# Kernel tuning notes

Measured on AMD Instinct MI355X. Metric: run time of the kernel, lower is better.

## Reference

```python
import jax, jax.numpy as jnp
import numpy as np

N = 50000      # nodes
E = 800000     # edges (before self-loops)
F_IN = 128     # args.nsegment
H = 4          # args.nhead
C = 32         # args.dhidden
OUT = 64       # output_dim
G = 64         # number of graphs in batch
NEG = 0.2      # args.negslope (and GATv2 internal leaky-relu slope, PyG default 0.2)


def setup_inputs() -> dict:
    key = jax.random.key(0)
    ks = jax.random.split(key, 8)
    def w(k, i, o):
        return jax.random.normal(k, (i, o), jnp.float32) / np.sqrt(i)
    x = jax.random.normal(ks[0], (N, F_IN), jnp.float32)
    edge_index = jax.random.randint(ks[1], (2, E), 0, N, dtype=jnp.int32)
    batch = jnp.sort(jax.random.randint(ks[2], (N,), 0, G, dtype=jnp.int32))
    d = dict(x=x, edge_index=edge_index, batch=batch)
    # layer dims: (in_dim, heads, out_per_head, concat)
    dims = [(F_IN, H, C, True), (H * C, H, C, True), (H * C, 1, OUT, False)]
    for li, (fi, h, c, concat) in enumerate(dims):
        k1, k2, k3 = jax.random.split(ks[3 + li], 3)
        d[f"Wl{li}"] = w(k1, fi, h * c)
        d[f"Wr{li}"] = w(k2, fi, h * c)
        d[f"att{li}"] = jax.random.normal(k3, (h, c), jnp.float32) / np.sqrt(c)
        d[f"b{li}"] = jnp.zeros((h * c if concat else c,), jnp.float32)
    return d


def _gat_layer(x, src, tgt, Wl, Wr, att, b, concat):
    """GATv2Conv: e_ij = att . leaky_relu(Wl x_j + Wr x_i); softmax over edges into i;
    out_i = sum_j alpha_ij * (Wl x_j). src/tgt include self-loops."""
    n = x.shape[0]
    h, c = att.shape
    xl = (x @ Wl).reshape(n, h, c)                 # source transform [N,h,c]
    xr = (x @ Wr).reshape(n, h, c)                 # target transform [N,h,c]
    g = jax.nn.leaky_relu(xl[src] + xr[tgt], NEG)  # [Etot,h,c]
    score = jnp.einsum('ehc,hc->eh', g, att)       # [Etot,h]
    smax = jax.ops.segment_max(score, tgt, num_segments=n)
    ex = jnp.exp(score - smax[tgt])
    den = jax.ops.segment_sum(ex, tgt, num_segments=n)
    alpha = ex / den[tgt]                          # per-target softmax [Etot,h]
    out = jax.ops.segment_sum(xl[src] * alpha[:, :, None], tgt, num_segments=n)
    out = out.reshape(n, h * c) if concat else out.mean(axis=1)
    return out + b


def _forward(x, edge_index, batch, params):
    n = x.shape[0]
    loops = jnp.arange(n, dtype=edge_index.dtype)  # PyG add_self_loops=True
    src = jnp.concatenate([edge_index[0], loops])
    tgt = jnp.concatenate([edge_index[1], loops])
    for Wl, Wr, att, b, concat in params:
        x = _gat_layer(x, src, tgt, Wl, Wr, att, b, concat)
        x = jax.nn.leaky_relu(x, NEG)  # dropout p is identity in eval mode
    ssum = jax.ops.segment_sum(x, batch, num_segments=G)
    cnt = jax.ops.segment_sum(jnp.ones((n,), x.dtype), batch, num_segments=G)
    return ssum / jnp.maximum(cnt, 1.0)[:, None]   # global_mean_pool -> [G, OUT]


def reference(x, edge_index, batch, Wl0, Wr0, att0, b0, Wl1, Wr1, att1, b1, Wl2, Wr2, att2, b2):
    params = [(Wl0, Wr0, att0, b0, True),
              (Wl1, Wr1, att1, b1, True),
              (Wl2, Wr2, att2, b2, False)]
    return _forward(x, edge_index, batch, params)
```

## Files before the change

### kernel.cpp

```cpp
#include <hip/hip_runtime.h>
#include <hip/hip_fp16.h>
#include <math.h>

#define NEGSLOPE 0.2f

typedef _Float16 f16x8 __attribute__((ext_vector_type(8)));
typedef float f32x4 __attribute__((ext_vector_type(4)));

__device__ __forceinline__ float lrelu(float x) { return x > 0.f ? x : NEGSLOPE * x; }

__global__ __launch_bounds__(256) void k_prep(
        const float* __restrict__ x, _Float16* __restrict__ xh, int n8, int XB,
        const float* W0, const float* W1, const float* W2,
        const float* W3, const float* W4, const float* W5,
        _Float16* D0, _Float16* D1, _Float16* D2,
        _Float16* D3, _Float16* D4, _Float16* D5,
        int* __restrict__ deg, float* __restrict__ pacc, int n, int npacc) {
    int b = blockIdx.x, t = threadIdx.x;
    if (b < XB) {
        int i = b * 256 + t;
        if (i < n8) {
            float4 a = ((const float4*)x)[2 * i], c = ((const float4*)x)[2 * i + 1];
            union { uint4 u; _Float16 h[8]; } pk;
            pk.h[0] = (_Float16)a.x; pk.h[1] = (_Float16)a.y;
            pk.h[2] = (_Float16)a.z; pk.h[3] = (_Float16)a.w;
            pk.h[4] = (_Float16)c.x; pk.h[5] = (_Float16)c.y;
            pk.h[6] = (_Float16)c.z; pk.h[7] = (_Float16)c.w;
            ((uint4*)xh)[i] = pk.u;
        }
    } else if (b < XB + 320) {
        const float* Ws[6] = {W0, W1, W2, W3, W4, W5};
        _Float16* Ds[6] = {D0, D1, D2, D3, D4, D5};
        int j = (b - XB) * 256 + t;
        int m, jj, kout;
        if (j < 65536) { m = j >> 14; jj = j & 16383; kout = 128; }
        else           { m = 4 + ((j - 65536) >> 13); jj = (j - 65536) & 8191; kout = 64; }
        int col = jj >> 7, k = jj & 127;
        Ds[m][col * 128 + k] = (_Float16)Ws[m][k * kout + col];
    } else {
        int i = (b - XB - 320) * 256 + t;
        if (i < n) deg[i] = 0;
        else if (i < n + npacc) pacc[i - n] = 0.f;
    }
}

__global__ void k_count(const int* __restrict__ tgt, int* __restrict__ deg,
                        int* __restrict__ rank, int e) {
    int i = blockIdx.x * 256 + threadIdx.x;
    if (i < e) rank[i] = atomicAdd(&deg[tgt[i]], 1);
}
__global__ __launch_bounds__(256) void k_scanA(const int* __restrict__ deg, int* __restrict__ rowptr,
                                               int* __restrict__ bsums, int n) {
    __shared__ int s[256];
    int t = threadIdx.x;
    int base = blockIdx.x * 4096 + t * 16;
    int pre[16];
    int sum = 0;
    for (int i = 0; i < 16; ++i) {
        int idx = base + i;
        int v = (idx < n) ? (deg[idx] + 1) : 0;
        pre[i] = sum;
        sum += v;
    }
    s[t] = sum;
    __syncthreads();
    for (int off = 1; off < 256; off <<= 1) {
        int v = (t >= off) ? s[t - off] : 0;
        __syncthreads();
        s[t] += v;
        __syncthreads();
    }
    int tbase = s[t] - sum;
    for (int i = 0; i < 16; ++i) {
        int idx = base + i;
        if (idx < n) rowptr[idx] = tbase + pre[i];
    }
    if (t == 0) bsums[blockIdx.x] = s[255];
}
__global__ __launch_bounds__(256) void k_scanC(int* __restrict__ rowptr, const int* __restrict__ bsums,
                                               int* __restrict__ edst, int nscan, int n) {
    __shared__ int pref[65];
    int t = threadIdx.x;
    if (t == 0) {
        int run = 0;
        for (int k = 0; k < nscan; ++k) { pref[k] = run; run += bsums[k]; }
        pref[nscan] = run;
    }
    __syncthreads();
    int i = blockIdx.x * 256 + t;
    if (i < n) {
        int rp = rowptr[i] + pref[i >> 12];
        rowptr[i] = rp;
        edst[rp] = i;
    }
    if (blockIdx.x == gridDim.x - 1 && t == 0) rowptr[n] = pref[nscan];
}
__global__ void k_scatter(const int* __restrict__ src, const int* __restrict__ tgt,
                          const int* __restrict__ rank, const int* __restrict__ rowptr,
                          int* __restrict__ edst, int e) {
    int i = blockIdx.x * 256 + threadIdx.x;
    if (i < e) {
        int p = rowptr[tgt[i]] + 1 + rank[i];
        __builtin_nontemporal_store(src[i], &edst[p]);
    }
}

template<int KOUT>
__global__ __launch_bounds__(256) void k_gemm_mfma(
        const _Float16* __restrict__ Ah,
        const _Float16* __restrict__ Wt0, const _Float16* __restrict__ Wt1,
        _Float16* __restrict__ out0, float* __restrict__ out1, int n) {
    constexpr int CT = KOUT / 16;
    int wv = threadIdx.x >> 6, lane = threadIdx.x & 63;
    int m = lane & 15, q = lane >> 4;
    int row0 = blockIdx.x * 64 + wv * 16;
    int arow = row0 + m; if (arow >= n) arow = n - 1;
    const _Float16* ap = Ah + (size_t)arow * 128 + q * 8;
    f16x8 af[4];
#pragma unroll
    for (int kt = 0; kt < 4; ++kt) af[kt] = *(const f16x8*)(ap + 32 * kt);

    f32x4 acc[2 * CT] = {};
#pragma unroll
    for (int kt = 0; kt < 4; ++kt) {
#pragma unroll
        for (int ct = 0; ct < 2 * CT; ++ct) {
            const _Float16* W = (ct < CT) ? Wt0 : Wt1;
            int col0 = (ct % CT) * 16;
            f16x8 bf = *(const f16x8*)(W + (size_t)(col0 + m) * 128 + 32 * kt + 8 * q);
            acc[ct] = __builtin_amdgcn_mfma_f32_16x16x32_f16(af[kt], bf, acc[ct], 0, 0, 0);
        }
    }
#pragma unroll
    for (int ct = 0; ct < 2 * CT; ++ct) {
        bool asHalf = (ct < CT);
        int col = (ct % CT) * 16 + m;
#pragma unroll
        for (int i = 0; i < 4; ++i) {
            int r = row0 + q * 4 + i;
            if (r < n) {
                if (asHalf) out0[(size_t)r * KOUT + col] = (_Float16)acc[ct][i];
                else        out1[(size_t)r * KOUT + col] = acc[ct][i];
            }
        }
    }
}

template<int H, int C, typename OutT>
__global__ __launch_bounds__(256) void k_agg(const __half* __restrict__ xl, const float* __restrict__ xr,
                                             const float* __restrict__ att, const float* __restrict__ bias,
                                             const int* __restrict__ rowptr, const int* __restrict__ edst,
                                             OutT* __restrict__ yout, int n) {
    constexpr int F = H * C;
    constexpr int VEC = F / 16;
    constexpr int L = C / VEC;
    int lane = threadIdx.x & 63;
    int wave = threadIdx.x >> 6;
    int s = lane & 15;
    int node = blockIdx.x * 16 + wave * 4 + (lane >> 4);
    bool valid = node < n;
    int nodeSafe = valid ? node : 0;
    int ch = s * VEC;

    float u[VEC], av[VEC], acc[VEC];
#pragma unroll
    for (int j = 0; j < VEC; ++j) {
        u[j] = xr[(size_t)nodeSafe * F + ch + j];
        av[j] = att[ch + j];
        acc[j] = 0.f;
    }
    int e0 = rowptr[nodeSafe];
    int deg = valid ? (rowptr[nodeSafe + 1] - e0) : 0;
    int maxdeg = deg;
    maxdeg = max(maxdeg, __shfl_xor(maxdeg, 16));
    maxdeg = max(maxdeg, __shfl_xor(maxdeg, 32));
    float ssum = 0.f;

    auto loadrow = [&](int src, float* v) {
        const __half* p = xl + (size_t)src * F + ch;
        if constexpr (VEC == 8) {
            union { uint4 u4; __half2 h[4]; } pk;
            pk.u4 = *(const uint4*)p;
#pragma unroll
            for (int j = 0; j < 4; ++j) {
                float2 f = __half22float2(pk.h[j]);
                v[2 * j] = f.x; v[2 * j + 1] = f.y;
            }
        } else {
            union { uint2 u2; __half2 h[2]; } pk;
            pk.u2 = *(const uint2*)p;
#pragma unroll
            for (int j = 0; j < 2; ++j) {
                float2 f = __half22float2(pk.h[j]);
                v[2 * j] = f.x; v[2 * j + 1] = f.y;
            }
        }
    };
    auto dot = [&](const float* v) {
        float p = 0.f;
#pragma unroll
        for (int j = 0; j < VEC; ++j) p += lrelu(v[j] + u[j]) * av[j];
        return p;
    };
    auto accum = [&](float w, const float* v) {
        ssum += w;
#pragma unroll
        for (int j = 0; j < VEC; ++j) acc[j] += w * v[j];
    };

    for (int base = 0; base < maxdeg; base += 16) {
        int cnt = deg - base;
        if (cnt > 16) cnt = 16;
        int idxreg = (s < cnt) ? edst[e0 + base + s] : nodeSafe;
        int mcnt = cnt;
        mcnt = max(mcnt, __shfl_xor(mcnt, 16));
        mcnt = max(mcnt, __shfl_xor(mcnt, 32));
        int gbase = lane & 48;
        int i = 0;
        for (; i + 4 <= mcnt; i += 4) {
            int s0 = __shfl(idxreg, gbase + i);
            int s1 = __shfl(idxreg, gbase + i + 1);
            int s2 = __shfl(idxreg, gbase + i + 2);
            int s3 = __shfl(idxreg, gbase + i + 3);
            float v0[VEC], v1[VEC], v2[VEC], v3[VEC];
            loadrow(s0, v0); loadrow(s1, v1); loadrow(s2, v2); loadrow(s3, v3);
            float p0 = dot(v0), p1 = dot(v1), p2 = dot(v2), p3 = dot(v3);
#pragma unroll
            for (int off = 1; off < L; off <<= 1) {
                p0 += __shfl_xor(p0, off);
                p1 += __shfl_xor(p1, off);
                p2 += __shfl_xor(p2, off);
                p3 += __shfl_xor(p3, off);
            }
            float w0 = (i + 0 < cnt) ? __expf(p0) : 0.f;
            float w1 = (i + 1 < cnt) ? __expf(p1) : 0.f;
            float w2 = (i + 2 < cnt) ? __expf(p2) : 0.f;
            float w3 = (i + 3 < cnt) ? __expf(p3) : 0.f;
            accum(w0, v0); accum(w1, v1); accum(w2, v2); accum(w3, v3);
        }
        for (; i < mcnt; ++i) {
            int s0 = __shfl(idxreg, gbase + i);
            float v[VEC];
            loadrow(s0, v);
            float p = dot(v);
#pragma unroll
            for (int off = 1; off < L; off <<= 1) p += __shfl_xor(p, off);
            float w = (i < cnt) ? __expf(p) : 0.f;
            accum(w, v);
        }
    }
    if (valid) {
        float inv = 1.f / ssum;
        float o[VEC];
#pragma unroll
        for (int j = 0; j < VEC; ++j) o[j] = lrelu(acc[j] * inv + bias[ch + j]);
        if constexpr (sizeof(OutT) == 2) {
            _Float16* p = (_Float16*)yout + (size_t)node * F + ch;
            if constexpr (VEC == 8) {
                union { uint4 u; _Float16 h[8]; } pk;
#pragma unroll
                for (int j = 0; j < 8; ++j) pk.h[j] = (_Float16)o[j];
                *(uint4*)p = pk.u;
            } else {
                union { uint2 u; _Float16 h[4]; } pk;
#pragma unroll
                for (int j = 0; j < 4; ++j) pk.h[j] = (_Float16)o[j];
                *(uint2*)p = pk.u;
            }
        } else {
            float* p = (float*)yout + (size_t)node * F + ch;
            *(float4*)p = make_float4(o[0], o[1], o[2], o[3]);
            if constexpr (VEC == 8)
                *(float4*)(p + 4) = make_float4(o[4], o[5], o[6], o[7]);
        }
    }
}

__global__ __launch_bounds__(256) void k_pool_partial(const float* __restrict__ y,
        const int* __restrict__ batch, float* __restrict__ pacc, int n, int nchunk) {
    __shared__ float sdata[256];
    __shared__ int range[2];
    int g = blockIdx.x;
    int chunk = blockIdx.y;
    int t = threadIdx.x;
    if (t == 0) {
        int lo = 0, hi = n;
        while (lo < hi) { int mid = (lo + hi) >> 1; if (batch[mid] < g) lo = mid + 1; else hi = mid; }
        range[0] = lo;
        hi = n;
        while (lo < hi) { int mid = (lo + hi) >> 1; if (batch[mid] < g + 1) lo = mid + 1; else hi = mid; }
        range[1] = lo;
    }
    __syncthreads();
    int start = range[0], len = range[1] - range[0];
    int lo = start + (int)((long long)len * chunk / nchunk);
    int hi = start + (int)((long long)len * (chunk + 1) / nchunk);
    int ch = t & 63, sub = t >> 6;
    float acc = 0.f;
    for (int node = lo + sub; node < hi; node += 4)
        acc += y[(size_t)node * 64 + ch];
    sdata[t] = acc;
    __syncthreads();
    if (t < 128) sdata[t] += sdata[t + 128];
    __syncthreads();
    if (t < 64) atomicAdd(&pacc[g * 64 + t], sdata[t] + sdata[t + 64]);
}
__global__ void k_pool_final(const float* __restrict__ pacc, const int* __restrict__ batch,
                             float* __restrict__ out, int n) {
    __shared__ int cntS;
    int g = blockIdx.x, t = threadIdx.x;
    if (t == 0) {
        int lo = 0, hi = n;
        while (lo < hi) { int mid = (lo + hi) >> 1; if (batch[mid] < g) lo = mid + 1; else hi = mid; }
        int s = lo;
        hi = n;
        while (lo < hi) { int mid = (lo + hi) >> 1; if (batch[mid] < g + 1) lo = mid + 1; else hi = mid; }
        cntS = lo - s;
    }
    __syncthreads();
    out[g * 64 + t] = pacc[g * 64 + t] / fmaxf((float)cntS, 1.f);
}

extern "C" void kernel_launch(void* const* d_in, const int* in_sizes, int n_in,
                              void* d_out, int out_size, void* d_ws, size_t ws_size,
                              hipStream_t stream) {
    const float* x     = (const float*)d_in[0];
    const int*   ei    = (const int*)d_in[1];
    const int*   batch = (const int*)d_in[2];
    const float* Wl0 = (const float*)d_in[3];
    const float* Wr0 = (const float*)d_in[4];
    const float* att0 = (const float*)d_in[5];
    const float* b0  = (const float*)d_in[6];
    const float* Wl1 = (const float*)d_in[7];
    const float* Wr1 = (const float*)d_in[8];
    const float* att1 = (const float*)d_in[9];
    const float* b1  = (const float*)d_in[10];
    const float* Wl2 = (const float*)d_in[11];
    const float* Wr2 = (const float*)d_in[12];
    const float* att2 = (const float*)d_in[13];
    const float* b2  = (const float*)d_in[14];

    const int N = in_sizes[2];
    const int E = in_sizes[1] / 2;
    const int G = out_size / 64;
    const int* src = ei;
    const int* tgt = ei + E;

    size_t off = 0;
    auto take = [&](size_t bytes) {
        void* p = (char*)d_ws + off;
        off = (off + bytes + 255) & ~(size_t)255;
        return p;
    };
    _Float16* xh   = (_Float16*)take((size_t)N * 128 * 2);
    _Float16* Ah   = (_Float16*)take((size_t)N * 128 * 2);
    float* B       = (float*)take((size_t)N * 128 * 4);
    _Float16* Cbh  = (_Float16*)take((size_t)N * 128 * 2);
    float* Cbf     = (float*)take((size_t)N * 64 * 4);
    _Float16* Wl0t = (_Float16*)take(128 * 128 * 2);
    _Float16* Wr0t = (_Float16*)take(128 * 128 * 2);
    _Float16* Wl1t = (_Float16*)take(128 * 128 * 2);
    _Float16* Wr1t = (_Float16*)take(128 * 128 * 2);
    _Float16* Wl2t = (_Float16*)take(64 * 128 * 2);
    _Float16* Wr2t = (_Float16*)take(64 * 128 * 2);
    int* rowptr = (int*)take((size_t)(N + 1) * 4);
    int* tmp    = (int*)take((size_t)N * 4);
    float* pacc = (float*)take((size_t)G * 64 * 4);
    int* rank   = (int*)take((size_t)E * 4);
    int* edst   = (int*)take((size_t)(E + N) * 4);
    int* bsums  = (int*)take(64 * 4);
    (void)ws_size; (void)n_in;

    const int TB = 256;
    int nblkN = (N + TB - 1) / TB;
    int nblkE = (E + TB - 1) / TB;
    int nscan = (N + 4095) / 4096;

    int n8 = N * 128 / 8;
    int XB = (n8 + TB - 1) / TB;
    int ZB = (N + G * 64 + TB - 1) / TB;
    k_prep<<<XB + 320 + ZB, TB, 0, stream>>>(x, xh, n8, XB,
        Wl0, Wr0, Wl1, Wr1, Wl2, Wr2,
        Wl0t, Wr0t, Wl1t, Wr1t, Wl2t, Wr2t,
        tmp, pacc, N, G * 64);

    k_count<<<nblkE, TB, 0, stream>>>(tgt, tmp, rank, E);
    k_scanA<<<nscan, TB, 0, stream>>>(tmp, rowptr, bsums, N);
    k_scanC<<<nblkN, TB, 0, stream>>>(rowptr, bsums, edst, nscan, N);
    k_scatter<<<nblkE, TB, 0, stream>>>(src, tgt, rank, rowptr, edst, E);

    int gemmBlocks = (N + 63) / 64;
    int aggBlocks = (N + 15) / 16;

    k_gemm_mfma<128><<<gemmBlocks, TB, 0, stream>>>(xh, Wl0t, Wr0t, Ah, B, N);
    k_agg<4, 32, _Float16><<<aggBlocks, TB, 0, stream>>>((const __half*)Ah, B, att0, b0, rowptr, edst, Cbh, N);

    k_gemm_mfma<128><<<gemmBlocks, TB, 0, stream>>>(Cbh, Wl1t, Wr1t, Ah, B, N);
    k_agg<4, 32, _Float16><<<aggBlocks, TB, 0, stream>>>((const __half*)Ah, B, att1, b1, rowptr, edst, Cbh, N);

    k_gemm_mfma<64><<<gemmBlocks, TB, 0, stream>>>(Cbh, Wl2t, Wr2t, Ah, B, N);
    k_agg<1, 64, float><<<aggBlocks, TB, 0, stream>>>((const __half*)Ah, B, att2, b2, rowptr, edst, Cbf, N);

    dim3 poolGrid(G, 16);
    k_pool_partial<<<poolGrid, TB, 0, stream>>>(Cbf, batch, pacc, N, 16);
    k_pool_final<<<G, 64, 0, stream>>>(pacc, batch, (float*)d_out, N);
}
```

Measured before the change: 404.1 us.

## Store target transform in fp16 and split GEMM columns across grid y

The target-side transform xr (B) is now written and read as fp16 instead of fp32, which halves that buffer's write traffic in the GEMM and its read traffic in the aggregation kernel. For the 128-wide layers the GEMM grid gains a y dimension of 2, so each block computes either Wl or Wr with 8 accumulator tiles instead of 16. This gives more blocks and lower register pressure, at the cost of re-reading the A tile. B fragments are also loaded into a register array before the MFMA loop, and the reduced xr precision can slightly perturb attention scores.

```diff
diff --git a/kernel.cpp b/kernel.cpp
--- a/kernel.cpp
+++ b/kernel.cpp
@@ -109,8 +109,7 @@
 __global__ __launch_bounds__(256) void k_gemm_mfma(
         const _Float16* __restrict__ Ah,
         const _Float16* __restrict__ Wt0, const _Float16* __restrict__ Wt1,
-        _Float16* __restrict__ out0, float* __restrict__ out1, int n) {
-    constexpr int CT = KOUT / 16;
+        _Float16* __restrict__ out0, _Float16* __restrict__ out1, int n) {
     int wv = threadIdx.x >> 6, lane = threadIdx.x & 63;
     int m = lane & 15, q = lane >> 4;
     int row0 = blockIdx.x * 64 + wv * 16;
@@ -120,34 +119,38 @@
 #pragma unroll
     for (int kt = 0; kt < 4; ++kt) af[kt] = *(const f16x8*)(ap + 32 * kt);
 
-    f32x4 acc[2 * CT] = {};
+    const _Float16* Wp = Wt0;
+    _Float16* outp = out0;
+    if (KOUT == 128 && blockIdx.y) { Wp = Wt1; outp = out1; }
+
+    f32x4 acc[8] = {};
 #pragma unroll
     for (int kt = 0; kt < 4; ++kt) {
-#pragma unroll
-        for (int ct = 0; ct < 2 * CT; ++ct) {
-            const _Float16* W = (ct < CT) ? Wt0 : Wt1;
-            int col0 = (ct % CT) * 16;
-            f16x8 bf = *(const f16x8*)(W + (size_t)(col0 + m) * 128 + 32 * kt + 8 * q);
-            acc[ct] = __builtin_amdgcn_mfma_f32_16x16x32_f16(af[kt], bf, acc[ct], 0, 0, 0);
-        }
-    }
-#pragma unroll
-    for (int ct = 0; ct < 2 * CT; ++ct) {
-        bool asHalf = (ct < CT);
-        int col = (ct % CT) * 16 + m;
+        f16x8 bfr[8];
+#pragma unroll
+        for (int ct = 0; ct < 8; ++ct) {
+            const _Float16* W = (KOUT == 128) ? Wp : (ct < 4 ? Wt0 : Wt1);
+            int col0 = (KOUT == 128) ? ct * 16 : (ct & 3) * 16;
+            bfr[ct] = *(const f16x8*)(W + (size_t)(col0 + m) * 128 + 32 * kt + 8 * q);
+        }
+#pragma unroll
+        for (int ct = 0; ct < 8; ++ct)
+            acc[ct] = __builtin_amdgcn_mfma_f32_16x16x32_f16(af[kt], bfr[ct], acc[ct], 0, 0, 0);
+    }
+#pragma unroll
+    for (int ct = 0; ct < 8; ++ct) {
+        _Float16* dst = (KOUT == 128) ? outp : (ct < 4 ? out0 : out1);
+        int col = ((KOUT == 128) ? ct * 16 : (ct & 3) * 16) + m;
 #pragma unroll
         for (int i = 0; i < 4; ++i) {
             int r = row0 + q * 4 + i;
-            if (r < n) {
-                if (asHalf) out0[(size_t)r * KOUT + col] = (_Float16)acc[ct][i];
-                else        out1[(size_t)r * KOUT + col] = acc[ct][i];
-            }
+            if (r < n) dst[(size_t)r * KOUT + col] = (_Float16)acc[ct][i];
         }
     }
 }
 
 template<int H, int C, typename OutT>
-__global__ __launch_bounds__(256) void k_agg(const __half* __restrict__ xl, const float* __restrict__ xr,
+__global__ __launch_bounds__(256) void k_agg(const __half* __restrict__ xl, const __half* __restrict__ xr,
                                              const float* __restrict__ att, const float* __restrict__ bias,
                                              const int* __restrict__ rowptr, const int* __restrict__ edst,
                                              OutT* __restrict__ yout, int n) {
@@ -162,22 +165,8 @@
     int nodeSafe = valid ? node : 0;
     int ch = s * VEC;
 
-    float u[VEC], av[VEC], acc[VEC];
-#pragma unroll
-    for (int j = 0; j < VEC; ++j) {
-        u[j] = xr[(size_t)nodeSafe * F + ch + j];
-        av[j] = att[ch + j];
-        acc[j] = 0.f;
-    }
-    int e0 = rowptr[nodeSafe];
-    int deg = valid ? (rowptr[nodeSafe + 1] - e0) : 0;
-    int maxdeg = deg;
-    maxdeg = max(maxdeg, __shfl_xor(maxdeg, 16));
-    maxdeg = max(maxdeg, __shfl_xor(maxdeg, 32));
-    float ssum = 0.f;
-
-    auto loadrow = [&](int src, float* v) {
-        const __half* p = xl + (size_t)src * F + ch;
+    auto loadrow = [&](const __half* base, int row, float* v) {
+        const __half* p = base + (size_t)row * F + ch;
         if constexpr (VEC == 8) {
             union { uint4 u4; __half2 h[4]; } pk;
             pk.u4 = *(const uint4*)p;
@@ -196,6 +185,21 @@
             }
         }
     };
+
+    float u[VEC], av[VEC], acc[VEC];
+    loadrow(xr, nodeSafe, u);
+#pragma unroll
+    for (int j = 0; j < VEC; ++j) {
+        av[j] = att[ch + j];
+        acc[j] = 0.f;
+    }
+    int e0 = rowptr[nodeSafe];
+    int deg = valid ? (rowptr[nodeSafe + 1] - e0) : 0;
+    int maxdeg = deg;
+    maxdeg = max(maxdeg, __shfl_xor(maxdeg, 16));
+    maxdeg = max(maxdeg, __shfl_xor(maxdeg, 32));
+    float ssum = 0.f;
+
     auto dot = [&](const float* v) {
         float p = 0.f;
 #pragma unroll
@@ -223,7 +227,8 @@
             int s2 = __shfl(idxreg, gbase + i + 2);
             int s3 = __shfl(idxreg, gbase + i + 3);
             float v0[VEC], v1[VEC], v2[VEC], v3[VEC];
-            loadrow(s0, v0); loadrow(s1, v1); loadrow(s2, v2); loadrow(s3, v3);
+            loadrow(xl, s0, v0); loadrow(xl, s1, v1);
+            loadrow(xl, s2, v2); loadrow(xl, s3, v3);
             float p0 = dot(v0), p1 = dot(v1), p2 = dot(v2), p3 = dot(v3);
 #pragma unroll
             for (int off = 1; off < L; off <<= 1) {
@@ -241,7 +246,7 @@
         for (; i < mcnt; ++i) {
             int s0 = __shfl(idxreg, gbase + i);
             float v[VEC];
-            loadrow(s0, v);
+            loadrow(xl, s0, v);
             float p = dot(v);
 #pragma unroll
             for (int off = 1; off < L; off <<= 1) p += __shfl_xor(p, off);
@@ -354,7 +359,7 @@
     };
     _Float16* xh   = (_Float16*)take((size_t)N * 128 * 2);
     _Float16* Ah   = (_Float16*)take((size_t)N * 128 * 2);
-    float* B       = (float*)take((size_t)N * 128 * 4);
+    _Float16* B    = (_Float16*)take((size_t)N * 128 * 2);
     _Float16* Cbh  = (_Float16*)take((size_t)N * 128 * 2);
     float* Cbf     = (float*)take((size_t)N * 64 * 4);
     _Float16* Wl0t = (_Float16*)take(128 * 128 * 2);
@@ -390,16 +395,18 @@
     k_scatter<<<nblkE, TB, 0, stream>>>(src, tgt, rank, rowptr, edst, E);
 
     int gemmBlocks = (N + 63) / 64;
+    dim3 gemmGrid2(gemmBlocks, 2);
+    dim3 gemmGrid1(gemmBlocks, 1);
     int aggBlocks = (N + 15) / 16;
 
-    k_gemm_mfma<128><<<gemmBlocks, TB, 0, stream>>>(xh, Wl0t, Wr0t, Ah, B, N);
-    k_agg<4, 32, _Float16><<<aggBlocks, TB, 0, stream>>>((const __half*)Ah, B, att0, b0, rowptr, edst, Cbh, N);
-
-    k_gemm_mfma<128><<<gemmBlocks, TB, 0, stream>>>(Cbh, Wl1t, Wr1t, Ah, B, N);
-    k_agg<4, 32, _Float16><<<aggBlocks, TB, 0, stream>>>((const __half*)Ah, B, att1, b1, rowptr, edst, Cbh, N);
-
-    k_gemm_mfma<64><<<gemmBlocks, TB, 0, stream>>>(Cbh, Wl2t, Wr2t, Ah, B, N);
-    k_agg<1, 64, float><<<aggBlocks, TB, 0, stream>>>((const __half*)Ah, B, att2, b2, rowptr, edst, Cbf, N);
+    k_gemm_mfma<128><<<gemmGrid2, TB, 0, stream>>>(xh, Wl0t, Wr0t, Ah, B, N);
+    k_agg<4, 32, _Float16><<<aggBlocks, TB, 0, stream>>>((const __half*)Ah, (const __half*)B, att0, b0, rowptr, edst, Cbh, N);
+
+    k_gemm_mfma<128><<<gemmGrid2, TB, 0, stream>>>(Cbh, Wl1t, Wr1t, Ah, B, N);
+    k_agg<4, 32, _Float16><<<aggBlocks, TB, 0, stream>>>((const __half*)Ah, (const __half*)B, att1, b1, rowptr, edst, Cbh, N);
+
+    k_gemm_mfma<64><<<gemmGrid1, TB, 0, stream>>>(Cbh, Wl2t, Wr2t, Ah, B, N);
+    k_agg<1, 64, float><<<aggBlocks, TB, 0, stream>>>((const __half*)Ah, (const __half*)B, att2, b2, rowptr, edst, Cbf, N);
 
     dim3 poolGrid(G, 16);
     k_pool_partial<<<poolGrid, TB, 0, stream>>>(Cbf, batch, pacc, N, 16);
```

New measurement: 380.6 us. 5.8% less time.
